# Kernel tuning notes

Measured on AMD Instinct MI355X. Metric: run time of the kernel, lower is better.

Reference implementation:

```python
import jax, jax.numpy as jnp
import numpy as np

EMBED, HEADS, LEVELS, POINTS, MLP = 256, 8, 3, 4, 4
SHAPES = [(60, 80), (30, 40), (15, 20)]  # (H, W) per level


def layer_norm(x, g, b):
    m = jnp.mean(x, -1, keepdims=True)
    v = jnp.mean((x - m) ** 2, -1, keepdims=True)
    return (x - m) * jax.lax.rsqrt(v + 1e-5) * g + b


def _bilinear(v, H, W, gx, gy):
    # v: [B,h,H*W,dh]; gx,gy: [B,h,Nq,P] absolute pixel coords (grid_sample align_corners=False, zero padding)
    x0 = jnp.floor(gx); y0 = jnp.floor(gy)
    wx = gx - x0; wy = gy - y0

    def g(xi, yi):
        valid = ((xi >= 0) & (xi < W) & (yi >= 0) & (yi < H)).astype(v.dtype)
        idx = jnp.clip(yi, 0, H - 1) * W + jnp.clip(xi, 0, W - 1)
        B, h, Nq, P = idx.shape
        out = jnp.take_along_axis(v, idx.reshape(B, h, Nq * P)[..., None], axis=2)
        return out.reshape(B, h, Nq, P, -1) * valid[..., None]

    x0i = x0.astype(jnp.int32); y0i = y0.astype(jnp.int32)
    return (g(x0i, y0i) * ((1 - wx) * (1 - wy))[..., None]
            + g(x0i + 1, y0i) * (wx * (1 - wy))[..., None]
            + g(x0i, y0i + 1) * ((1 - wx) * wy)[..., None]
            + g(x0i + 1, y0i + 1) * (wx * wy)[..., None])


def setup_inputs() -> dict:
    key = jax.random.key(0)
    ks = jax.random.split(key, 16)
    B, Nq, C = 2, 8192, EMBED
    Nv = sum(h * w for h, w in SHAPES)
    s = 0.02
    d = {
        'query': jax.random.normal(ks[0], (B, Nq, C), jnp.float32),
        'value': jax.random.normal(ks[1], (B, Nv, C), jnp.float32),
        'query_pos': jax.random.normal(ks[2], (B, Nq, C), jnp.float32),
        'ref_pts': jax.random.uniform(ks[3], (B, Nq, LEVELS, 2), jnp.float32),
        'spatial_shapes': jnp.array(SHAPES, jnp.int32),
        'level_start_index': jnp.array(np.cumsum([0] + [h * w for h, w in SHAPES[:-1]]), jnp.int32),
        'g1': jnp.ones((C,), jnp.float32), 'b1': jnp.zeros((C,), jnp.float32),
        'Wo': s * jax.random.normal(ks[4], (C, HEADS * LEVELS * POINTS * 2), jnp.float32),
        'bo': jnp.zeros((HEADS * LEVELS * POINTS * 2,), jnp.float32),
        'Wa': s * jax.random.normal(ks[5], (C, HEADS * LEVELS * POINTS), jnp.float32),
        'ba': jnp.zeros((HEADS * LEVELS * POINTS,), jnp.float32),
        'Wv': s * jax.random.normal(ks[6], (C, C), jnp.float32), 'bv': jnp.zeros((C,), jnp.float32),
        'Wp': s * jax.random.normal(ks[7], (C, C), jnp.float32), 'bp': jnp.zeros((C,), jnp.float32),
        'g2': jnp.ones((C,), jnp.float32), 'b2': jnp.zeros((C,), jnp.float32),
        'Wf1': s * jax.random.normal(ks[8], (C, MLP * C), jnp.float32), 'bf1': jnp.zeros((MLP * C,), jnp.float32),
        'Wf2': s * jax.random.normal(ks[9], (MLP * C, C), jnp.float32), 'bf2': jnp.zeros((C,), jnp.float32),
    }
    return d


def reference(query, value, query_pos, ref_pts, spatial_shapes, level_start_index,
              g1, b1, Wo, bo, Wa, ba, Wv, bv, Wp, bp, g2, b2, Wf1, bf1, Wf2, bf2):
    B, Nq, C = query.shape
    dh = C // HEADS
    shapes = np.asarray(spatial_shapes).tolist()
    starts = np.asarray(level_start_index).tolist()

    qn = layer_norm(query, g1, b1)           # pre-norm
    qa = qn + query_pos                       # positional embedding inside attn
    offs = (qa @ Wo + bo).reshape(B, Nq, HEADS, LEVELS, POINTS, 2)
    aw = jax.nn.softmax((qa @ Wa + ba).reshape(B, Nq, HEADS, LEVELS * POINTS), -1)
    aw = aw.reshape(B, Nq, HEADS, LEVELS, POINTS)
    v = (value @ Wv + bv).reshape(B, -1, HEADS, dh).transpose(0, 2, 1, 3)  # [B,h,Nv,dh]

    # offset_normalizer = (W, H) per level
    norm = jnp.array([[w, h] for h, w in shapes], jnp.float32)
    loc = ref_pts[:, :, None, :, None, :] + offs / norm[None, None, None, :, None, :]

    out = jnp.zeros((B, Nq, HEADS, dh), query.dtype)
    for l, (H, W) in enumerate(shapes):
        vl = jax.lax.dynamic_slice_in_dim(v, starts[l], H * W, axis=2)
        gl = loc[:, :, :, l].transpose(0, 2, 1, 3, 4)   # [B,h,Nq,P,2]
        gx = gl[..., 0] * W - 0.5
        gy = gl[..., 1] * H - 0.5
        sampled = _bilinear(vl, H, W, gx, gy)            # [B,h,Nq,P,dh]
        out = out + jnp.einsum('bhqpd,bqhp->bqhd', sampled, aw[:, :, :, l])

    attn = out.reshape(B, Nq, C) @ Wp + bp + qn          # output proj + mmcv internal residual (identity=norm1(query))
    q = query + attn                                     # layer residual
    q2 = layer_norm(q, g2, b2)
    return q + (jax.nn.gelu(q2 @ Wf1 + bf1, approximate=False) @ Wf2 + bf2)
```

## Files before the change

### kernel.cpp

```cpp
#include <hip/hip_runtime.h>
#include <math.h>


typedef short short8 __attribute__((ext_vector_type(8)));
typedef short s16x4 __attribute__((ext_vector_type(4)));
typedef __bf16 bf16x8 __attribute__((ext_vector_type(8)));
typedef float f32x4 __attribute__((ext_vector_type(4)));

#if defined(__has_attribute)
#if __has_attribute(amdgpu_num_vgpr)
#define WPMLP_REGS __attribute__((amdgpu_num_vgpr(128)))
#else
#define WPMLP_REGS
#endif
#else
#define WPMLP_REGS
#endif

__device__ __forceinline__ short f2b(float f) {
  unsigned u = __builtin_bit_cast(unsigned, f);
  u += 0x7fffu + ((u >> 16) & 1u);
  return (short)(u >> 16);
}
__device__ __forceinline__ float b2f(short s) {
  unsigned u = ((unsigned)(unsigned short)s) << 16;
  return __builtin_bit_cast(float, u);
}
__device__ __forceinline__ void b8f(short8 s, float* f) {
  const uint4 u = __builtin_bit_cast(uint4, s);
  f[0] = __builtin_bit_cast(float, u.x << 16);
  f[1] = __builtin_bit_cast(float, u.x & 0xffff0000u);
  f[2] = __builtin_bit_cast(float, u.y << 16);
  f[3] = __builtin_bit_cast(float, u.y & 0xffff0000u);
  f[4] = __builtin_bit_cast(float, u.z << 16);
  f[5] = __builtin_bit_cast(float, u.z & 0xffff0000u);
  f[6] = __builtin_bit_cast(float, u.w << 16);
  f[7] = __builtin_bit_cast(float, u.w & 0xffff0000u);
}

__device__ __forceinline__ f32x4 mfma16(short8 a, short8 b, f32x4 c) {
  return __builtin_amdgcn_mfma_f32_16x16x32_bf16(
      __builtin_bit_cast(bf16x8, a), __builtin_bit_cast(bf16x8, b), c, 0, 0, 0);
}

typedef __attribute__((address_space(3))) unsigned int lds_u32;
typedef const __attribute__((address_space(1))) unsigned int glb_u32;
__device__ __forceinline__ void glds16(const void* g, void* l) {
  __builtin_amdgcn_global_load_lds((glb_u32*)g, (lds_u32*)l, 16, 0, 0);
}

__device__ __forceinline__ float gelu1(float v) {
  return 0.5f * v * (1.f + erff(v * 0.70710678118654752f));
}

template <int EPI>
__device__ __forceinline__ void gemm64_core(
    int bx, int by,
    const short* __restrict__ A, const short* __restrict__ Bt,
    const float* __restrict__ bias, const float* __restrict__ bias2,
    void* __restrict__ Cout, int M, int Nreal, int ldc, int K, char* smem)
{
  short* sA = (short*)smem;
  short* sB = sA + 4096;
  float* sf = (float*)smem;

  const int t = threadIdx.x;
  const int wave = t >> 6, lane = t & 63;
  const int quad = lane >> 4, l16 = lane & 15;
  const int wm = (wave & 1) * 32, wn = (wave >> 1) * 64;
  const int m0 = by * 64, n0 = bx * 128;

  f32x4 acc[2][4];
#pragma unroll
  for (int i = 0; i < 2; i++)
#pragma unroll
    for (int j = 0; j < 4; j++) acc[i][j] = (f32x4){0.f, 0.f, 0.f, 0.f};

  const int srow = lane >> 3, pos = lane & 7;
  const int chunk = (pos + srow) & 7;
  const short* gA = A + (size_t)(m0 + wave * 16 + srow) * K + chunk * 8;
  const short* gB = Bt + (size_t)(n0 + wave * 32 + srow) * K + chunk * 8;

  const int nk = K >> 6;
  for (int kt = 0; kt < nk; ++kt) {
    if (kt) __syncthreads();
    const int ko = kt * 64;
#pragma unroll
    for (int g = 0; g < 2; ++g)
      glds16(gA + ko + (size_t)(g * 8) * K, sA + (wave * 16 + g * 8) * 64);
#pragma unroll
    for (int g = 0; g < 4; ++g)
      glds16(gB + ko + (size_t)(g * 8) * K, sB + (wave * 32 + g * 8) * 64);
    __syncthreads();
#pragma unroll
    for (int kk = 0; kk < 2; ++kk) {
      short8 af[2], bf[4];
      const int c = kk * 4 + quad;
#pragma unroll
      for (int i = 0; i < 2; i++) {
        const int lrA = wm + i * 16 + l16;
        af[i] = *(const short8*)&sA[lrA * 64 + ((c - lrA) & 7) * 8];
      }
#pragma unroll
      for (int j = 0; j < 4; j++) {
        const int lrB = wn + j * 16 + l16;
        bf[j] = *(const short8*)&sB[lrB * 64 + ((c - lrB) & 7) * 8];
      }
#pragma unroll
      for (int i = 0; i < 2; i++)
#pragma unroll
        for (int j = 0; j < 4; j++) acc[i][j] = mfma16(bf[j], af[i], acc[i][j]);
    }
  }
  __syncthreads();

#pragma unroll
  for (int b = 0; b < 2; ++b) {
    if (wm == b * 32) {
#pragma unroll
      for (int i = 0; i < 2; ++i) {
        const int rr = i * 16 + l16;
#pragma unroll
        for (int j = 0; j < 4; ++j)
          *(f32x4*)&sf[rr * 132 + wn + quad * 4 + j * 16] = acc[i][j];
      }
    }
    __syncthreads();
#pragma unroll
    for (int r2 = 0; r2 < 4; ++r2) {
      const int fidx = r2 * 1024 + t * 4;
      const int row = fidx >> 7, col = fidx & 127;
      const int gm = m0 + b * 32 + row;
      const int cc = n0 + col;
      if (gm < M && cc < Nreal) {
        const float4 v = *(const float4*)&sf[row * 132 + col];
        float4 bb;
        if (EPI == 4) bb = (cc < 192) ? *(const float4*)(bias + cc)
                                      : *(const float4*)(bias2 + cc - 192);
        else bb = *(const float4*)(bias + cc);
        float v0 = v.x + bb.x, v1 = v.y + bb.y, v2 = v.z + bb.z, v3 = v.w + bb.w;
        s16x4 o; o.x = f2b(v0); o.y = f2b(v1); o.z = f2b(v2); o.w = f2b(v3);
        *(s16x4*)((short*)Cout + (size_t)gm * ldc + cc) = o;
      }
    }
    __syncthreads();
  }
}

__global__ __launch_bounds__(256) void gemm_oa_v(
    const short* __restrict__ qa, const short* __restrict__ wt_oa,
    const float* __restrict__ bo, const float* __restrict__ ba,
    short* __restrict__ oabuf,
    const short* __restrict__ valbf, const short* __restrict__ wt_v,
    const float* __restrict__ bv, short* __restrict__ vproj)
{
  __shared__ __align__(16) char smem[24576];
  const int idx = blockIdx.x;
  if (idx < 768) {
    gemm64_core<4>(idx % 3, idx / 3, qa, wt_oa, bo, ba,
                   oabuf, 16384, 288, 288, 256, smem);
  } else {
    const int r = idx - 768;
    gemm64_core<5>(r % 2, r / 2, valbf, wt_v, bv, nullptr,
                   vproj, 12600, 256, 256, 256, smem);
  }
}

__global__ __launch_bounds__(1024) WPMLP_REGS void wp_mlp(
    const short* __restrict__ sampled,
    const short* __restrict__ wtp,
    const float* __restrict__ bp,
    const short* __restrict__ qnb,
    const float* __restrict__ query,
    const float* __restrict__ g2, const float* __restrict__ b2v,
    const short* __restrict__ wf1,
    const float* __restrict__ b1v,
    const short* __restrict__ wf2,
    const float* __restrict__ bf2v,
    float* __restrict__ outp)
{
  __shared__ __align__(16) char smem[131072];
  float* Q  = (float*)smem;
  short* H  = (short*)(smem + 65536);
  short* RA = (short*)(smem + 98304);

  const int t = threadIdx.x;
  const int w = t >> 6, lane = t & 63;
  const int quad = lane >> 4, l16 = lane & 15;
  const int wm2 = w >> 3, wn8 = w & 7;
  const int m0 = blockIdx.x * 64;

#pragma unroll
  for (int qq = 0; qq < 2; ++qq) {
    const int g = qq * 1024 + t;
    const int row = g >> 5, p = g & 31;
    const int cl = (p & ~7) | ((p + row) & 7);
    glds16(sampled + (size_t)(m0 + row) * 256 + cl * 8,
           RA + (qq * 1024 + w * 64) * 8);
  }
  __syncthreads();

  {
    f32x4 accp[2][2];
#pragma unroll
    for (int i = 0; i < 2; i++)
#pragma unroll
      for (int j = 0; j < 2; j++) accp[i][j] = (f32x4){0.f, 0.f, 0.f, 0.f};
#pragma unroll
    for (int kk = 0; kk < 8; ++kk) {
      const int c = kk * 4 + quad;
      short8 afr[2], bfr[2];
#pragma unroll
      for (int i = 0; i < 2; ++i) {
        const int r = wm2 * 32 + i * 16 + l16;
        const int pos = (c & ~7) | ((c - r) & 7);
        afr[i] = *(const short8*)(RA + r * 256 + pos * 8);
      }
#pragma unroll
      for (int j = 0; j < 2; ++j) {
        const int n1 = wn8 * 2 + j;
        bfr[j] = *(const short8*)(wtp + ((size_t)n1 * 32 + c) * 128 + l16 * 8);
      }
#pragma unroll
      for (int i = 0; i < 2; ++i)
#pragma unroll
        for (int j = 0; j < 2; ++j) accp[i][j] = mfma16(bfr[j], afr[i], accp[i][j]);
    }
#pragma unroll
    for (int i = 0; i < 2; ++i)
#pragma unroll
      for (int j = 0; j < 2; ++j) {
        const int r = wm2 * 32 + i * 16 + l16;
        const int cc = wn8 * 32 + j * 16 + quad * 4;
        *(f32x4*)&Q[r * 256 + (cc ^ ((r & 7) << 2))] = accp[i][j];
      }
  }
  __syncthreads();

  {
    const float4 bbp  = *(const float4*)(bp + lane * 4);
    const float4 gv   = *(const float4*)(g2 + lane * 4);
    const float4 bb2  = *(const float4*)(b2v + lane * 4);
#pragma unroll
    for (int rep = 0; rep < 4; ++rep) {
      const int row = rep * 16 + w;
      const int gm = m0 + row;
      const int cs = (lane * 4) ^ ((row & 7) << 2);
      const float4 a  = *(const float4*)&Q[row * 256 + cs];
      const float4 qv = *(const float4*)(query + (size_t)gm * 256 + lane * 4);
      const s16x4 qn  = *(const s16x4*)(qnb + (size_t)gm * 256 + lane * 4);
      float v0 = a.x + bbp.x + b2f(qn.x) + qv.x;
      float v1 = a.y + bbp.y + b2f(qn.y) + qv.y;
      float v2 = a.z + bbp.z + b2f(qn.z) + qv.z;
      float v3 = a.w + bbp.w + b2f(qn.w) + qv.w;
      float s = v0 + v1 + v2 + v3;
#pragma unroll
      for (int o = 32; o; o >>= 1) s += __shfl_xor(s, o);
      const float mean = s * (1.f / 256.f);
      const float d0 = v0 - mean, d1 = v1 - mean, d2 = v2 - mean, d3 = v3 - mean;
      float ss = d0 * d0 + d1 * d1 + d2 * d2 + d3 * d3;
#pragma unroll
      for (int o = 32; o; o >>= 1) ss += __shfl_xor(ss, o);
      const float inv = rsqrtf(ss * (1.f / 256.f) + 1e-5f);
      *(f32x4*)&Q[row * 256 + cs] = (f32x4){v0, v1, v2, v3};
      const int col = lane * 4;
      const int c = col >> 3;
      const int pos = (c & ~7) | ((c - row) & 7);
      s16x4 o2;
      o2.x = f2b(d0 * inv * gv.x + bb2.x);
      o2.y = f2b(d1 * inv * gv.y + bb2.y);
      o2.z = f2b(d2 * inv * gv.z + bb2.z);
      o2.w = f2b(d3 * inv * gv.w + bb2.w);
      *(s16x4*)(RA + row * 256 + pos * 8 + (col & 7)) = o2;
    }
  }
  __syncthreads();

  f32x4 acc2[2][2];
#pragma unroll
  for (int i = 0; i < 2; i++)
#pragma unroll
    for (int j = 0; j < 2; j++) acc2[i][j] = (f32x4){0.f, 0.f, 0.f, 0.f};

  for (int q = 0; q < 4; ++q) {
    if (q) __syncthreads();
    f32x4 acc1[2][2];
#pragma unroll
    for (int i = 0; i < 2; i++)
#pragma unroll
      for (int j = 0; j < 2; j++) acc1[i][j] = (f32x4){0.f, 0.f, 0.f, 0.f};
#pragma unroll
    for (int kk = 0; kk < 8; ++kk) {
      const int cg = kk * 4 + quad;
      short8 afr[2], bfr[2];
#pragma unroll
      for (int i = 0; i < 2; ++i) {
        const int r = wm2 * 32 + i * 16 + l16;
        const int pos = (cg & ~7) | ((cg - r) & 7);
        afr[i] = *(const short8*)(RA + r * 256 + pos * 8);
      }
#pragma unroll
      for (int j = 0; j < 2; ++j) {
        const int n1 = q * 16 + wn8 * 2 + j;
        bfr[j] = *(const short8*)(wf1 + ((size_t)n1 * 32 + cg) * 128 + l16 * 8);
      }
#pragma unroll
      for (int i = 0; i < 2; ++i)
#pragma unroll
        for (int j = 0; j < 2; ++j) acc1[i][j] = mfma16(bfr[j], afr[i], acc1[i][j]);
    }
#pragma unroll
    for (int j = 0; j < 2; ++j) {
      const int coll = wn8 * 32 + j * 16 + quad * 4;
      const float4 bb = *(const float4*)(b1v + q * 256 + coll);
      const int c = coll >> 3;
#pragma unroll
      for (int i = 0; i < 2; ++i) {
        const int r = wm2 * 32 + i * 16 + l16;
        const int pos = (c & ~7) | ((c - r) & 7);
        s16x4 o;
        o.x = f2b(gelu1(acc1[i][j].x + bb.x));
        o.y = f2b(gelu1(acc1[i][j].y + bb.y));
        o.z = f2b(gelu1(acc1[i][j].z + bb.z));
        o.w = f2b(gelu1(acc1[i][j].w + bb.w));
        *(s16x4*)(H + r * 256 + pos * 8 + (coll & 7)) = o;
      }
    }
    __syncthreads();

#pragma unroll 4
    for (int kk = 0; kk < 8; ++kk) {
      const int cl = kk * 4 + quad;
      short8 afr[2], bfr[2];
#pragma unroll
      for (int i = 0; i < 2; ++i) {
        const int r = wm2 * 32 + i * 16 + l16;
        const int pos = (cl & ~7) | ((cl - r) & 7);
        afr[i] = *(const short8*)(H + r * 256 + pos * 8);
      }
#pragma unroll
      for (int j = 0; j < 2; ++j) {
        const int n1 = wn8 * 2 + j;
        bfr[j] = *(const short8*)(wf2 + ((size_t)n1 * 128 + q * 32 + cl) * 128 + l16 * 8);
      }
#pragma unroll
      for (int i = 0; i < 2; ++i)
#pragma unroll
        for (int j = 0; j < 2; ++j) acc2[i][j] = mfma16(bfr[j], afr[i], acc2[i][j]);
    }
  }

  {
#pragma unroll
    for (int i = 0; i < 2; ++i)
#pragma unroll
      for (int j = 0; j < 2; ++j) {
        const int r = wm2 * 32 + i * 16 + l16;
        const int cc = wn8 * 32 + j * 16 + quad * 4;
        const int cs = cc ^ ((r & 7) << 2);
        const float4 bb = *(const float4*)(bf2v + cc);
        const float4 qb = *(const float4*)&Q[r * 256 + cs];
        *(f32x4*)&Q[r * 256 + cs] =
            (f32x4){qb.x + acc2[i][j].x + bb.x, qb.y + acc2[i][j].y + bb.y,
                    qb.z + acc2[i][j].z + bb.z, qb.w + acc2[i][j].w + bb.w};
      }
  }
  __syncthreads();

#pragma unroll
  for (int rep = 0; rep < 4; ++rep) {
    const int row = rep * 16 + w;
    const int gm = m0 + row;
    const int cs = (lane * 4) ^ ((row & 7) << 2);
    const float4 v = *(const float4*)&Q[row * 256 + cs];
    *(float4*)(outp + (size_t)gm * 256 + lane * 4) = v;
  }
}

__global__ __launch_bounds__(256) void prep_all(
    const float* __restrict__ Wo, const float* __restrict__ Wa,
    const float* __restrict__ Wv, const float* __restrict__ Wp,
    const float* __restrict__ Wf1, const float* __restrict__ Wf2,
    short* __restrict__ t_oa, short* __restrict__ t_v, short* __restrict__ t_p,
    short* __restrict__ t_f1, short* __restrict__ t_f2,
    const float* __restrict__ value, short* __restrict__ valbf,
    const float* __restrict__ query, const float* __restrict__ query_pos,
    const float* __restrict__ g1, const float* __restrict__ b1,
    short* __restrict__ qnb, short* __restrict__ qa)
{
  __shared__ float tile[32][33];
  const int t = threadIdx.x;
  const int blk = blockIdx.x;

  if (blk < 1792) {
    const int bxa = blk & 255, bya = blk >> 8;
    int K, N, noff; const float* src; short* dst;
    switch (bya) {
      case 0: src = Wo;      dst = t_oa; K = 256;  N = 192;  noff = 0;   break;
      case 1: src = Wa;      dst = t_oa; K = 256;  N = 96;   noff = 192; break;
      case 2: src = nullptr; dst = t_oa; K = 256;  N = 96;   noff = 288; break;
      case 3: src = Wv;      dst = t_v;  K = 256;  N = 256;  noff = 0;   break;
      case 4: src = Wp;      dst = t_p;  K = 256;  N = 256;  noff = 0;   break;
      case 5: src = Wf1;     dst = t_f1; K = 256;  N = 1024; noff = 0;   break;
      default: src = Wf2;    dst = t_f2; K = 1024; N = 256;  noff = 0;   break;
    }
    const bool fragpack = (bya >= 4);
    const int tilesK = K >> 5;
    const int nt = tilesK * (N >> 5);
    if (bxa >= nt) return;
    const int tk = bxa % tilesK, tn = bxa / tilesK;
    const int k0 = tk * 32, n0 = tn * 32;
    const int r = t >> 3, c4 = (t & 7) * 4;
    float4 v = make_float4(0.f, 0.f, 0.f, 0.f);
    if (src) v = *(const float4*)(src + (size_t)(k0 + r) * N + n0 + c4);
    tile[r][c4] = v.x; tile[r][c4 + 1] = v.y; tile[r][c4 + 2] = v.z; tile[r][c4 + 3] = v.w;
    __syncthreads();
    const int nn = t >> 3, kc = (t & 7) * 4;
    s16x4 o;
    o.x = f2b(tile[kc][nn]); o.y = f2b(tile[kc + 1][nn]);
    o.z = f2b(tile[kc + 2][nn]); o.w = f2b(tile[kc + 3][nn]);
    if (fragpack) {
      const int n = n0 + nn, k = k0 + kc;
      *(s16x4*)(dst + ((size_t)(n >> 4) * (K >> 3) + (k >> 3)) * 128 +
                (n & 15) * 8 + (k & 7)) = o;
    } else {
      *(s16x4*)(dst + (size_t)(noff + n0 + nn) * K + k0 + kc) = o;
    }
  } else if (blk < 1792 + 3169) {
    const int i = ((blk - 1792) * 256 + t) * 4;
    if (i >= 12672 * 256) return;
    s16x4 o = (s16x4){0, 0, 0, 0};
    if (i < 12600 * 256) {
      float4 v = *(const float4*)(value + i);
      o.x = f2b(v.x); o.y = f2b(v.y); o.z = f2b(v.z); o.w = f2b(v.w);
    }
    *(s16x4*)(valbf + i) = o;
  } else {
    const int row  = (blk - 4961) * 4 + (t >> 6);
    const int lane = t & 63;
    const float4 v = ((const float4*)(query + (size_t)row * 256))[lane];
    float s = v.x + v.y + v.z + v.w;
#pragma unroll
    for (int o = 32; o; o >>= 1) s += __shfl_xor(s, o);
    const float mean = s * (1.f / 256.f);
    const float dx = v.x - mean, dy = v.y - mean, dz = v.z - mean, dw = v.w - mean;
    float s2 = dx * dx + dy * dy + dz * dz + dw * dw;
#pragma unroll
    for (int o = 32; o; o >>= 1) s2 += __shfl_xor(s2, o);
    const float inv = rsqrtf(s2 * (1.f / 256.f) + 1e-5f);
    const float4 gv = ((const float4*)g1)[lane];
    const float4 bv = ((const float4*)b1)[lane];
    const float4 o1 = make_float4(dx * inv * gv.x + bv.x, dy * inv * gv.y + bv.y,
                                  dz * inv * gv.z + bv.z, dw * inv * gv.w + bv.w);
    s16x4 ob; ob.x = f2b(o1.x); ob.y = f2b(o1.y); ob.z = f2b(o1.z); ob.w = f2b(o1.w);
    ((s16x4*)(qnb + (size_t)row * 256))[lane] = ob;
    const float4 pv = ((const float4*)(query_pos + (size_t)row * 256))[lane];
    s16x4 op;
    op.x = f2b(o1.x + pv.x); op.y = f2b(o1.y + pv.y);
    op.z = f2b(o1.z + pv.z); op.w = f2b(o1.w + pv.w);
    ((s16x4*)(qa + (size_t)row * 256))[lane] = op;
  }
}

__global__ __launch_bounds__(256) void deform_fused(
    const short* __restrict__ vproj, const short* __restrict__ oa,
    const float* __restrict__ refp, short* __restrict__ out)
{
  __shared__ int4 sIdx[768];
  __shared__ s16x4 sW[768];
  const int t = threadIdx.x;

  if (t < 64) {
    const int row = blockIdx.x * 8 + (t >> 3), h = t & 7;
    const short* oarow = oa + (size_t)row * 288;
    float off[24];
    {
      const short8* op = (const short8*)(oarow + h * 24);
      b8f(op[0], off); b8f(op[1], off + 8); b8f(op[2], off + 16);
    }
    float lg[12];
    {
      const s16x4* ap = (const s16x4*)(oarow + 192 + h * 12);
#pragma unroll
      for (int i = 0; i < 3; i++) {
        const s16x4 v = ap[i];
        lg[i * 4] = b2f(v.x); lg[i * 4 + 1] = b2f(v.y);
        lg[i * 4 + 2] = b2f(v.z); lg[i * 4 + 3] = b2f(v.w);
      }
    }
    const float* rp = refp + (size_t)row * 6;
    const float Rx[3] = {rp[0], rp[2], rp[4]}, Ry[3] = {rp[1], rp[3], rp[5]};
    float mx = lg[0];
#pragma unroll
    for (int i = 1; i < 12; i++) mx = fmaxf(mx, lg[i]);
    float sum = 0.f;
#pragma unroll
    for (int i = 0; i < 12; i++) { lg[i] = __expf(lg[i] - mx); sum += lg[i]; }
    const float inv = 1.f / sum;
    const int b = row >> 13;
    const int Hs[3] = {60, 30, 15}, Ws[3] = {80, 40, 20}, St[3] = {0, 4800, 6000};
#pragma unroll
    for (int p = 0; p < 12; p++) {
      const int l = p >> 2;
      const int W = Ws[l], H = Hs[l];
      const float gx = Rx[l] * W + off[p * 2]     - 0.5f;
      const float gy = Ry[l] * H + off[p * 2 + 1] - 0.5f;
      const float x0f = floorf(gx), y0f = floorf(gy);
      const float wx = gx - x0f, wy = gy - y0f;
      const int x0 = (int)x0f, y0 = (int)y0f;
      const float aw = lg[p] * inv;
      float cw[4] = {(1.f - wx) * (1.f - wy), wx * (1.f - wy),
                     (1.f - wx) * wy, wx * wy};
      const int base = b * 6300 + St[l];
      int ci[4];
#pragma unroll
      for (int k = 0; k < 4; k++) {
        const int xx = x0 + (k & 1), yy = y0 + (k >> 1);
        const bool valid = (xx >= 0) & (xx < W) & (yy >= 0) & (yy < H);
        const int xc = min(max(xx, 0), W - 1);
        const int yc = min(max(yy, 0), H - 1);
        ci[k] = ((base + yc * W + xc) << 8) + h * 32;
        cw[k] = valid ? cw[k] * aw : 0.f;
      }
      sIdx[t * 12 + p] = make_int4(ci[0], ci[1], ci[2], ci[3]);
      s16x4 wv; wv.x = f2b(cw[0]); wv.y = f2b(cw[1]); wv.z = f2b(cw[2]); wv.w = f2b(cw[3]);
      sW[t * 12 + p] = wv;
    }
  }
  __syncthreads();

  const int lu = t >> 2, c4 = (t & 3) * 8;
  float acc[8];
#pragma unroll
  for (int i = 0; i < 8; i++) acc[i] = 0.f;
#pragma unroll 2
  for (int p = 0; p < 12; p++) {
    const int4 idx = sIdx[lu * 12 + p];
    const s16x4 wb = sW[lu * 12 + p];
    const float w0 = b2f(wb.x), w1 = b2f(wb.y), w2 = b2f(wb.z), w3 = b2f(wb.w);
    const short8 v0 = *(const short8*)(vproj + idx.x + c4);
    const short8 v1 = *(const short8*)(vproj + idx.y + c4);
    const short8 v2 = *(const short8*)(vproj + idx.z + c4);
    const short8 v3 = *(const short8*)(vproj + idx.w + c4);
    float f0[8], f1[8], f2[8], f3[8];
    b8f(v0, f0); b8f(v1, f1); b8f(v2, f2); b8f(v3, f3);
#pragma unroll
    for (int j = 0; j < 8; j++)
      acc[j] += w0 * f0[j] + w1 * f1[j] + w2 * f2[j] + w3 * f3[j];
  }
  short8 o;
#pragma unroll
  for (int j = 0; j < 8; j++) o[j] = f2b(acc[j]);
  *(short8*)(out + (size_t)(blockIdx.x * 256 + t) * 8) = o;
}

extern "C" void kernel_launch(void* const* d_in, const int* in_sizes, int n_in,
                              void* d_out, int out_size, void* d_ws, size_t ws_size,
                              hipStream_t stream)
{
  const float* query     = (const float*)d_in[0];
  const float* value     = (const float*)d_in[1];
  const float* query_pos = (const float*)d_in[2];
  const float* ref_pts   = (const float*)d_in[3];
  const float* g1  = (const float*)d_in[6];
  const float* b1  = (const float*)d_in[7];
  const float* Wo  = (const float*)d_in[8];
  const float* bo  = (const float*)d_in[9];
  const float* Wa  = (const float*)d_in[10];
  const float* ba  = (const float*)d_in[11];
  const float* Wv  = (const float*)d_in[12];
  const float* bv  = (const float*)d_in[13];
  const float* Wp  = (const float*)d_in[14];
  const float* bp  = (const float*)d_in[15];
  const float* g2  = (const float*)d_in[16];
  const float* b2  = (const float*)d_in[17];
  const float* Wf1 = (const float*)d_in[18];
  const float* bf1 = (const float*)d_in[19];
  const float* Wf2 = (const float*)d_in[20];
  const float* bf2 = (const float*)d_in[21];

  char* ws = (char*)d_ws;
  short* wt_oa   = (short*)(ws + 0);
  short* wt_v    = (short*)(ws + 196608);
  short* wt_p    = (short*)(ws + 327680);
  short* wt_f1   = (short*)(ws + 458752);
  short* wt_f2   = (short*)(ws + 983040);
  short* qnb     = (short*)(ws + 1507328);
  short* qa      = (short*)(ws + 18284544);
  short* oabuf   = (short*)(ws + 26673152);
  short* vproj   = (short*)(ws + 45547520);
  short* sampled = (short*)(ws + 51998720);
  short* valbf   = (short*)(ws + 77164544);
  float* outp = (float*)d_out;

  prep_all<<<9057, 256, 0, stream>>>(Wo, Wa, Wv, Wp, Wf1, Wf2,
                                     wt_oa, wt_v, wt_p, wt_f1, wt_f2,
                                     value, valbf, query, query_pos,
                                     g1, b1, qnb, qa);
  gemm_oa_v<<<1162, 256, 0, stream>>>(qa, wt_oa, bo, ba, oabuf,
                                      valbf, wt_v, bv, vproj);
  deform_fused<<<2048, 256, 0, stream>>>(vproj, oabuf, ref_pts, sampled);
  wp_mlp<<<256, 1024, 0, stream>>>(sampled, wt_p, bp, qnb, query, g2, b2,
                                   wt_f1, bf1, wt_f2, bf2, outp);
}
```

Before: 206.9 us.

## Replace tiled offset/attn and value-projection GEMM with full-N row-block kernel

The old 64x128 tiled GEMM, which staged both A and B through LDS over K-loops, is replaced by a 1024-thread kernel. Each block loads a whole 64x256 A row-block into LDS once and computes every output column, reading B fragments straight from global memory in a fragment-packed layout. The prep kernel now writes all weights in that packed layout, so each B fragment is a contiguous 16-byte load. Outputs are staged in LDS for coalesced row stores. The launch drops from 1162 to 453 blocks and the repeated A loads across column tiles go away, at the cost of B reads coming from global/L2 instead of LDS and fewer, larger blocks. The register cap attribute on wp_mlp is also removed.

Result: no change. 208.8 us (+0.9%).

```diff
diff --git a/kernel.cpp b/kernel.cpp
--- a/kernel.cpp
+++ b/kernel.cpp
@@ -6,16 +6,6 @@
 typedef short s16x4 __attribute__((ext_vector_type(4)));
 typedef __bf16 bf16x8 __attribute__((ext_vector_type(8)));
 typedef float f32x4 __attribute__((ext_vector_type(4)));
-
-#if defined(__has_attribute)
-#if __has_attribute(amdgpu_num_vgpr)
-#define WPMLP_REGS __attribute__((amdgpu_num_vgpr(128)))
-#else
-#define WPMLP_REGS
-#endif
-#else
-#define WPMLP_REGS
-#endif
 
 __device__ __forceinline__ short f2b(float f) {
   unsigned u = __builtin_bit_cast(unsigned, f);
@@ -53,120 +43,133 @@
   return 0.5f * v * (1.f + erff(v * 0.70710678118654752f));
 }
 
-template <int EPI>
-__device__ __forceinline__ void gemm64_core(
-    int bx, int by,
-    const short* __restrict__ A, const short* __restrict__ Bt,
-    const float* __restrict__ bias, const float* __restrict__ bias2,
-    void* __restrict__ Cout, int M, int Nreal, int ldc, int K, char* smem)
-{
-  short* sA = (short*)smem;
-  short* sB = sA + 4096;
-  float* sf = (float*)smem;
-
-  const int t = threadIdx.x;
-  const int wave = t >> 6, lane = t & 63;
-  const int quad = lane >> 4, l16 = lane & 15;
-  const int wm = (wave & 1) * 32, wn = (wave >> 1) * 64;
-  const int m0 = by * 64, n0 = bx * 128;
-
-  f32x4 acc[2][4];
-#pragma unroll
-  for (int i = 0; i < 2; i++)
-#pragma unroll
-    for (int j = 0; j < 4; j++) acc[i][j] = (f32x4){0.f, 0.f, 0.f, 0.f};
-
-  const int srow = lane >> 3, pos = lane & 7;
-  const int chunk = (pos + srow) & 7;
-  const short* gA = A + (size_t)(m0 + wave * 16 + srow) * K + chunk * 8;
-  const short* gB = Bt + (size_t)(n0 + wave * 32 + srow) * K + chunk * 8;
-
-  const int nk = K >> 6;
-  for (int kt = 0; kt < nk; ++kt) {
-    if (kt) __syncthreads();
-    const int ko = kt * 64;
-#pragma unroll
-    for (int g = 0; g < 2; ++g)
-      glds16(gA + ko + (size_t)(g * 8) * K, sA + (wave * 16 + g * 8) * 64);
-#pragma unroll
-    for (int g = 0; g < 4; ++g)
-      glds16(gB + ko + (size_t)(g * 8) * K, sB + (wave * 32 + g * 8) * 64);
-    __syncthreads();
-#pragma unroll
-    for (int kk = 0; kk < 2; ++kk) {
-      short8 af[2], bf[4];
-      const int c = kk * 4 + quad;
-#pragma unroll
-      for (int i = 0; i < 2; i++) {
-        const int lrA = wm + i * 16 + l16;
-        af[i] = *(const short8*)&sA[lrA * 64 + ((c - lrA) & 7) * 8];
-      }
-#pragma unroll
-      for (int j = 0; j < 4; j++) {
-        const int lrB = wn + j * 16 + l16;
-        bf[j] = *(const short8*)&sB[lrB * 64 + ((c - lrB) & 7) * 8];
-      }
-#pragma unroll
-      for (int i = 0; i < 2; i++)
-#pragma unroll
-        for (int j = 0; j < 4; j++) acc[i][j] = mfma16(bf[j], af[i], acc[i][j]);
-    }
-  }
-  __syncthreads();
-
-#pragma unroll
-  for (int b = 0; b < 2; ++b) {
-    if (wm == b * 32) {
-#pragma unroll
-      for (int i = 0; i < 2; ++i) {
-        const int rr = i * 16 + l16;
-#pragma unroll
-        for (int j = 0; j < 4; ++j)
-          *(f32x4*)&sf[rr * 132 + wn + quad * 4 + j * 16] = acc[i][j];
-      }
-    }
-    __syncthreads();
-#pragma unroll
-    for (int r2 = 0; r2 < 4; ++r2) {
-      const int fidx = r2 * 1024 + t * 4;
-      const int row = fidx >> 7, col = fidx & 127;
-      const int gm = m0 + b * 32 + row;
-      const int cc = n0 + col;
-      if (gm < M && cc < Nreal) {
-        const float4 v = *(const float4*)&sf[row * 132 + col];
-        float4 bb;
-        if (EPI == 4) bb = (cc < 192) ? *(const float4*)(bias + cc)
-                                      : *(const float4*)(bias2 + cc - 192);
-        else bb = *(const float4*)(bias + cc);
-        float v0 = v.x + bb.x, v1 = v.y + bb.y, v2 = v.z + bb.z, v3 = v.w + bb.w;
-        s16x4 o; o.x = f2b(v0); o.y = f2b(v1); o.z = f2b(v2); o.w = f2b(v3);
-        *(s16x4*)((short*)Cout + (size_t)gm * ldc + cc) = o;
-      }
-    }
-    __syncthreads();
-  }
-}
-
-__global__ __launch_bounds__(256) void gemm_oa_v(
+__global__ __launch_bounds__(1024) void gemm_oa_v2(
     const short* __restrict__ qa, const short* __restrict__ wt_oa,
     const float* __restrict__ bo, const float* __restrict__ ba,
     short* __restrict__ oabuf,
     const short* __restrict__ valbf, const short* __restrict__ wt_v,
     const float* __restrict__ bv, short* __restrict__ vproj)
 {
-  __shared__ __align__(16) char smem[24576];
-  const int idx = blockIdx.x;
-  if (idx < 768) {
-    gemm64_core<4>(idx % 3, idx / 3, qa, wt_oa, bo, ba,
-                   oabuf, 16384, 288, 288, 256, smem);
+  __shared__ __align__(16) char smem[70144];
+  short* stg = (short*)smem;
+  short* RA  = (short*)(smem + 37376);
+
+  const int t = threadIdx.x;
+  const int w = t >> 6, lane = t & 63;
+  const int quad = lane >> 4, l16 = lane & 15;
+  const int wm2 = w >> 3, wn8 = w & 7;
+  const bool is_oa = blockIdx.x < 256;
+  const int m0 = (is_oa ? blockIdx.x : (blockIdx.x - 256)) * 64;
+  const short* A  = is_oa ? qa : valbf;
+  const short* wt = is_oa ? wt_oa : wt_v;
+
+#pragma unroll
+  for (int qq = 0; qq < 2; ++qq) {
+    const int g = qq * 1024 + t;
+    const int row = g >> 5, p = g & 31;
+    const int cl = (p & ~7) | ((p + row) & 7);
+    glds16(A + (size_t)(m0 + row) * 256 + cl * 8,
+           RA + (qq * 1024 + w * 64) * 8);
+  }
+  __syncthreads();
+
+  if (is_oa) {
+    f32x4 acc[2][3];
+#pragma unroll
+    for (int i = 0; i < 2; i++)
+#pragma unroll
+      for (int j = 0; j < 3; j++) acc[i][j] = (f32x4){0.f, 0.f, 0.f, 0.f};
+#pragma unroll
+    for (int kk = 0; kk < 8; ++kk) {
+      const int c = kk * 4 + quad;
+      short8 afr[2], bfr[3];
+#pragma unroll
+      for (int i = 0; i < 2; ++i) {
+        const int r = wm2 * 32 + i * 16 + l16;
+        const int pos = (c & ~7) | ((c - r) & 7);
+        afr[i] = *(const short8*)(RA + r * 256 + pos * 8);
+      }
+#pragma unroll
+      for (int j = 0; j < 3; ++j) {
+        const int n1 = wn8 * 3 + j;
+        bfr[j] = *(const short8*)(wt + ((size_t)n1 * 32 + c) * 128 + l16 * 8);
+      }
+#pragma unroll
+      for (int i = 0; i < 2; ++i)
+#pragma unroll
+        for (int j = 0; j < 3; ++j) acc[i][j] = mfma16(bfr[j], afr[i], acc[i][j]);
+    }
+#pragma unroll
+    for (int i = 0; i < 2; ++i)
+#pragma unroll
+      for (int j = 0; j < 3; ++j) {
+        const int col = (wn8 * 3 + j) * 16 + quad * 4;
+        if (col < 288) {
+          const int r = wm2 * 32 + i * 16 + l16;
+          const float4 bb = (col < 192) ? *(const float4*)(bo + col)
+                                        : *(const float4*)(ba + col - 192);
+          s16x4 o;
+          o.x = f2b(acc[i][j].x + bb.x); o.y = f2b(acc[i][j].y + bb.y);
+          o.z = f2b(acc[i][j].z + bb.z); o.w = f2b(acc[i][j].w + bb.w);
+          *(s16x4*)(stg + r * 292 + col) = o;
+        }
+      }
+    __syncthreads();
+    for (int e = t; e < 4608; e += 1024) {
+      const int row = e / 72, c4 = (e % 72) * 4;
+      *(s16x4*)(oabuf + (size_t)(m0 + row) * 288 + c4) =
+          *(const s16x4*)(stg + row * 292 + c4);
+    }
   } else {
-    const int r = idx - 768;
-    gemm64_core<5>(r % 2, r / 2, valbf, wt_v, bv, nullptr,
-                   vproj, 12600, 256, 256, 256, smem);
-  }
-}
-
-__global__ __launch_bounds__(1024) WPMLP_REGS void wp_mlp(
+    f32x4 acc[2][2];
+#pragma unroll
+    for (int i = 0; i < 2; i++)
+#pragma unroll
+      for (int j = 0; j < 2; j++) acc[i][j] = (f32x4){0.f, 0.f, 0.f, 0.f};
+#pragma unroll
+    for (int kk = 0; kk < 8; ++kk) {
+      const int c = kk * 4 + quad;
+      short8 afr[2], bfr[2];
+#pragma unroll
+      for (int i = 0; i < 2; ++i) {
+        const int r = wm2 * 32 + i * 16 + l16;
+        const int pos = (c & ~7) | ((c - r) & 7);
+        afr[i] = *(const short8*)(RA + r * 256 + pos * 8);
+      }
+#pragma unroll
+      for (int j = 0; j < 2; ++j) {
+        const int n1 = wn8 * 2 + j;
+        bfr[j] = *(const short8*)(wt + ((size_t)n1 * 32 + c) * 128 + l16 * 8);
+      }
+#pragma unroll
+      for (int i = 0; i < 2; ++i)
+#pragma unroll
+        for (int j = 0; j < 2; ++j) acc[i][j] = mfma16(bfr[j], afr[i], acc[i][j]);
+    }
+#pragma unroll
+    for (int i = 0; i < 2; ++i)
+#pragma unroll
+      for (int j = 0; j < 2; ++j) {
+        const int col = (wn8 * 2 + j) * 16 + quad * 4;
+        const int r = wm2 * 32 + i * 16 + l16;
+        const float4 bb = *(const float4*)(bv + col);
+        s16x4 o;
+        o.x = f2b(acc[i][j].x + bb.x); o.y = f2b(acc[i][j].y + bb.y);
+        o.z = f2b(acc[i][j].z + bb.z); o.w = f2b(acc[i][j].w + bb.w);
+        *(s16x4*)(stg + r * 268 + col) = o;
+      }
+    __syncthreads();
+    for (int e = t; e < 4096; e += 1024) {
+      const int row = e >> 6, c4 = (e & 63) * 4;
+      const int gm = m0 + row;
+      if (gm < 12600)
+        *(s16x4*)(vproj + (size_t)gm * 256 + c4) =
+            *(const s16x4*)(stg + row * 268 + c4);
+    }
+  }
+}
+
+__global__ __launch_bounds__(1024) void wp_mlp(
     const short* __restrict__ sampled,
     const short* __restrict__ wtp,
     const float* __restrict__ bp,
@@ -404,7 +407,6 @@
       case 5: src = Wf1;     dst = t_f1; K = 256;  N = 1024; noff = 0;   break;
       default: src = Wf2;    dst = t_f2; K = 1024; N = 256;  noff = 0;   break;
     }
-    const bool fragpack = (bya >= 4);
     const int tilesK = K >> 5;
     const int nt = tilesK * (N >> 5);
     if (bxa >= nt) return;
@@ -419,13 +421,9 @@
     s16x4 o;
     o.x = f2b(tile[kc][nn]); o.y = f2b(tile[kc + 1][nn]);
     o.z = f2b(tile[kc + 2][nn]); o.w = f2b(tile[kc + 3][nn]);
-    if (fragpack) {
-      const int n = n0 + nn, k = k0 + kc;
-      *(s16x4*)(dst + ((size_t)(n >> 4) * (K >> 3) + (k >> 3)) * 128 +
-                (n & 15) * 8 + (k & 7)) = o;
-    } else {
-      *(s16x4*)(dst + (size_t)(noff + n0 + nn) * K + k0 + kc) = o;
-    }
+    const int n = noff + n0 + nn, k = k0 + kc;
+    *(s16x4*)(dst + ((size_t)(n >> 4) * (K >> 3) + (k >> 3)) * 128 +
+              (n & 15) * 8 + (k & 7)) = o;
   } else if (blk < 1792 + 3169) {
     const int i = ((blk - 1792) * 256 + t) * 4;
     if (i >= 12672 * 256) return;
@@ -597,8 +595,8 @@
                                      wt_oa, wt_v, wt_p, wt_f1, wt_f2,
                                      value, valbf, query, query_pos,
                                      g1, b1, qnb, qa);
-  gemm_oa_v<<<1162, 256, 0, stream>>>(qa, wt_oa, bo, ba, oabuf,
-                                      valbf, wt_v, bv, vproj);
+  gemm_oa_v2<<<453, 1024, 0, stream>>>(qa, wt_oa, bo, ba, oabuf,
+                                       valbf, wt_v, bv, vproj);
   deform_fused<<<2048, 256, 0, stream>>>(vproj, oabuf, ref_pts, sampled);
   wp_mlp<<<256, 1024, 0, stream>>>(sampled, wt_p, bp, qnb, query, g2, b2,
                                    wt_f1, bf1, wt_f2, bf2, outp);
```
